# Kernel optimization log

Measured on AMD Instinct MI355X. Metric: run time of the kernel, lower is better.

The kernel has to match this reference:

```python
import jax, jax.numpy as jnp
import numpy as np

N, IN, HID, HEADS, OUT, E = 50000, 128, 64, 4, 128, 800000
NEG_SLOPE = 0.2


def _gat_conv(x, src, dst, W, a_src, a_dst, b, heads, ch, concat):
    # x: [N, F_in]; W: [F_in, heads*ch]; a_src/a_dst: [heads, ch]; b: [heads*ch] or [ch]
    n = x.shape[0]
    h = (x @ W).reshape(n, heads, ch)                       # [N,H,C]
    al_s = jnp.einsum('nhc,hc->nh', h, a_src)               # [N,H]
    al_d = jnp.einsum('nhc,hc->nh', h, a_dst)               # [N,H]
    e = jax.nn.leaky_relu(al_s[src] + al_d[dst], NEG_SLOPE)  # [E,H]
    # segment softmax over destination nodes (every node has a self-loop)
    m = jax.ops.segment_max(e, dst, num_segments=n)
    ex = jnp.exp(e - m[dst])
    denom = jax.ops.segment_sum(ex, dst, num_segments=n)
    alpha = ex / denom[dst]                                  # [E,H]
    msg = h[src] * alpha[:, :, None]                         # [E,H,C]
    out = jax.ops.segment_sum(msg, dst, num_segments=n)      # [N,H,C]
    out = out.reshape(n, heads * ch) if concat else out.mean(axis=1)
    return out + b


def setup_inputs() -> dict:
    key = jax.random.key(0)
    ks = jax.random.split(key, 10)
    s = 0.1
    return {
        'node_features': jax.random.normal(ks[0], (N, IN), jnp.float32),
        'edge_index': jax.random.randint(ks[1], (2, E), 0, N, jnp.int64),
        'W1': jax.random.normal(ks[2], (IN, HEADS * HID), jnp.float32) * s,
        'a1_src': jax.random.normal(ks[3], (HEADS, HID), jnp.float32) * s,
        'a1_dst': jax.random.normal(ks[4], (HEADS, HID), jnp.float32) * s,
        'b1': jnp.zeros((HEADS * HID,), jnp.float32),
        'W2': jax.random.normal(ks[5], (HEADS * HID, OUT), jnp.float32) * s,
        'a2_src': jax.random.normal(ks[6], (1, OUT), jnp.float32) * s,
        'a2_dst': jax.random.normal(ks[7], (1, OUT), jnp.float32) * s,
        'b2': jnp.zeros((OUT,), jnp.float32),
    }


def reference(node_features, edge_index, W1, a1_src, a1_dst, b1, W2, a2_src, a2_dst, b2):
    n = node_features.shape[0]
    loops = jnp.arange(n, dtype=edge_index.dtype)
    src = jnp.concatenate([edge_index[0], loops])  # PyG adds self-loops by default
    dst = jnp.concatenate([edge_index[1], loops])
    x = _gat_conv(node_features, src, dst, W1, a1_src, a1_dst, b1, HEADS, HID, True)
    x = jax.nn.relu(x)
    x = _gat_conv(x, src, dst, W2, a2_src, a2_dst, b2, 1, OUT, False)
    return x
```

## Files before the change

kernel.cpp:

```cpp
#include <hip/hip_runtime.h>
#include <math.h>

#define N_NODES 50000
#define F_IN    128
#define HIDC    64
#define HEADS   4
#define C1      (HEADS*HIDC)
#define F_OUT   128
#define NE      800000
#define NET     (NE + N_NODES)
#define NEG_SLOPE 0.2f

#define NPB   49
#define NBUCK 1021
#define BPAD  16
#define K4CAP 2048
#define SCHUNK 8192

typedef unsigned short ushort_t;
typedef signed char    schar_t;
typedef __attribute__((ext_vector_type(8))) short bf16x8;
typedef __attribute__((ext_vector_type(8))) unsigned short us8;
typedef __attribute__((ext_vector_type(4))) float f32x4;

__device__ __forceinline__ float b2f(ushort_t x) {
  return __uint_as_float(((unsigned int)x) << 16);
}
__device__ __forceinline__ ushort_t f2bf(float f) {
  unsigned int u = __float_as_uint(f);
  return (ushort_t)((u + 0x7fffu + ((u >> 16) & 1u)) >> 16);
}
__device__ __forceinline__ float u2f_lo(unsigned int u) { return __uint_as_float(u << 16); }
__device__ __forceinline__ float u2f_hi(unsigned int u) { return __uint_as_float(u & 0xffff0000u); }

__device__ __forceinline__ void fma8v(float ww, uint4 vv, float* a) {
  a[0] = fmaf(ww, u2f_lo(vv.x), a[0]); a[1] = fmaf(ww, u2f_hi(vv.x), a[1]);
  a[2] = fmaf(ww, u2f_lo(vv.y), a[2]); a[3] = fmaf(ww, u2f_hi(vv.y), a[3]);
  a[4] = fmaf(ww, u2f_lo(vv.z), a[4]); a[5] = fmaf(ww, u2f_hi(vv.z), a[5]);
  a[6] = fmaf(ww, u2f_lo(vv.w), a[6]); a[7] = fmaf(ww, u2f_hi(vv.w), a[7]);
}
__device__ __forceinline__ void fma8q(float wsc, uint2 vv, float* a) {
  int x = (int)vv.x, y = (int)vv.y;
  a[0] = fmaf(wsc, (float)(schar_t)(x),        a[0]);
  a[1] = fmaf(wsc, (float)(schar_t)(x >> 8),   a[1]);
  a[2] = fmaf(wsc, (float)(schar_t)(x >> 16),  a[2]);
  a[3] = fmaf(wsc, (float)(x >> 24),           a[3]);
  a[4] = fmaf(wsc, (float)(schar_t)(y),        a[4]);
  a[5] = fmaf(wsc, (float)(schar_t)(y >> 8),   a[5]);
  a[6] = fmaf(wsc, (float)(schar_t)(y >> 16),  a[6]);
  a[7] = fmaf(wsc, (float)(y >> 24),           a[7]);
}


__global__ __launch_bounds__(256) void bucket_count(const int* __restrict__ ei,
                                                    int* __restrict__ bcnt) {
  __shared__ int hist[NBUCK];
  for (int i = threadIdx.x; i < NBUCK; i += 256) hist[i] = 0;
  __syncthreads();
  int stride = gridDim.x * 256;
  for (int e = blockIdx.x * 256 + threadIdx.x; e < NET; e += stride) {
    int d = (e < NE) ? ei[NE + e] : (e - NE);
    atomicAdd(&hist[d / NPB], 1);
  }
  __syncthreads();
  for (int i = threadIdx.x; i < NBUCK; i += 256)
    if (hist[i]) atomicAdd(&bcnt[i * BPAD], hist[i]);
}

__global__ __launch_bounds__(1024) void scan_buckets(const int* __restrict__ bcnt,
                                                     int* __restrict__ boff) {
  __shared__ int sh[1024];
  int t = threadIdx.x;
  sh[t] = (t < NBUCK) ? bcnt[t * BPAD] : 0;
  __syncthreads();
#pragma unroll
  for (int off = 1; off < 1024; off <<= 1) {
    int u = (t >= off) ? sh[t - off] : 0;
    __syncthreads();
    sh[t] += u;
    __syncthreads();
  }
  if (t < NBUCK) boff[t + 1] = sh[t];
  if (t == 0) boff[0] = 0;
}

__global__ __launch_bounds__(1024) void bucket_scatter_blocked(const int* __restrict__ ei,
                                                               const int* __restrict__ boff,
                                                               int* __restrict__ bfill,
                                                               int2* __restrict__ pairs) {
  __shared__ int hist[NBUCK];
  __shared__ int gbase[NBUCK];
  __shared__ int fill[NBUCK];
  int c0 = blockIdx.x * SCHUNK;
  int cend = min(c0 + SCHUNK, NET);
  for (int i = threadIdx.x; i < NBUCK; i += 1024) { hist[i] = 0; fill[i] = 0; }
  __syncthreads();
  for (int e = c0 + threadIdx.x; e < cend; e += 1024) {
    int d = (e < NE) ? ei[NE + e] : (e - NE);
    atomicAdd(&hist[d / NPB], 1);
  }
  __syncthreads();
  for (int i = threadIdx.x; i < NBUCK; i += 1024)
    if (hist[i]) gbase[i] = boff[i] + atomicAdd(&bfill[i * BPAD], hist[i]);
  __syncthreads();
  for (int e = c0 + threadIdx.x; e < cend; e += 1024) {
    int s, d;
    if (e < NE) { s = ei[e]; d = ei[NE + e]; }
    else        { s = e - NE; d = s; }
    int b = d / NPB;
    int lpos = atomicAdd(&fill[b], 1);
    pairs[gbase[b] + lpos] = make_int2(s, d);
  }
}

__global__ __launch_bounds__(256) void build_csr(const int2* __restrict__ pairs,
                                                 const int* __restrict__ boff,
                                                 int* __restrict__ rowptr,
                                                 int* __restrict__ colsrc) {
  __shared__ int cnt[NPB];
  __shared__ int loc[NPB + 1];
  __shared__ int2 buf[K4CAP];
  int b = blockIdx.x, t = threadIdx.x;
  int p0 = boff[b], p1 = boff[b + 1];
  int m = p1 - p0;
  int n0 = b * NPB;
  int nn = min(NPB, N_NODES - n0);
  for (int i = t; i < NPB; i += 256) cnt[i] = 0;
  __syncthreads();
  bool inlds = (m <= K4CAP);
  for (int i = t; i < m; i += 256) {
    int2 p = pairs[p0 + i];
    if (inlds) buf[i] = p;
    atomicAdd(&cnt[p.y - n0], 1);
  }
  __syncthreads();
  if (t == 0) {
    int run = 0;
#pragma unroll 1
    for (int j = 0; j < nn; ++j) { loc[j] = run; run += cnt[j]; }
    loc[nn] = run;
  }
  __syncthreads();
  for (int j = t; j < nn; j += 256) rowptr[n0 + j] = p0 + loc[j];
  if (t == 0 && n0 + nn == N_NODES) rowptr[N_NODES] = NET;
  for (int i = t; i < NPB; i += 256) cnt[i] = 0;
  __syncthreads();
  for (int i = t; i < m; i += 256) {
    int2 p = inlds ? buf[i] : pairs[p0 + i];
    int j = p.y - n0;
    int pos = atomicAdd(&cnt[j], 1);
    colsrc[p0 + loc[j] + pos] = p.x;
  }
}


__global__ void transpose_both(const float* __restrict__ W1, ushort_t* __restrict__ W1t,
                               const float* __restrict__ W2, ushort_t* __restrict__ W2t) {
  int idx = blockIdx.x * blockDim.x + threadIdx.x;
  if (idx < F_IN * C1) {
    int k = idx / C1, n = idx - k * C1;
    W1t[(size_t)n * F_IN + k] = f2bf(W1[idx]);
  } else {
    int j = idx - F_IN * C1;
    if (j < C1 * F_OUT) {
      int k = j / F_OUT, n = j - k * F_OUT;
      W2t[(size_t)n * C1 + k] = f2bf(W2[j]);
    }
  }
}


#define BKS 64
#define LDT 72

__device__ __forceinline__ us8 stage8(const ushort_t* p) { return *(const us8*)p; }
__device__ __forceinline__ us8 stage8(const float* p) {
  float4 f0 = *(const float4*)p;
  float4 f1 = *(const float4*)(p + 4);
  us8 o;
  o[0] = f2bf(f0.x); o[1] = f2bf(f0.y); o[2] = f2bf(f0.z); o[3] = f2bf(f0.w);
  o[4] = f2bf(f1.x); o[5] = f2bf(f1.y); o[6] = f2bf(f1.z); o[7] = f2bf(f1.w);
  return o;
}

template<int K, int NCOL, int AL_MODE, typename AT, typename CT>
__global__ __launch_bounds__(256) void gemm_mfma(const AT* __restrict__ A,
                                                 const ushort_t* __restrict__ Bt,
                                                 CT* __restrict__ C,
                                                 float* __restrict__ scales,
                                                 const float* __restrict__ a_s,
                                                 const float* __restrict__ a_d,
                                                 float* __restrict__ als,
                                                 float* __restrict__ ald) {
  __shared__ __align__(16) char smem[2 * 128 * LDT * 2];
  ushort_t (*Asl)[LDT] = (ushort_t(*)[LDT])smem;
  ushort_t (*Bsl)[LDT] = (ushort_t(*)[LDT])(smem + 128 * LDT * 2);

  const int tid = threadIdx.x;
  const int lane = tid & 63;
  const int wave = tid >> 6;
  const int wr = wave >> 1, wc = wave & 1;
  const int row0 = blockIdx.y * 128;
  const int col0 = blockIdx.x * 128;
  const int l15 = lane & 15, l4 = lane >> 4;

  f32x4 acc[4][4] = {};

  for (int k0 = 0; k0 < K; k0 += BKS) {
#pragma unroll
    for (int i = 0; i < 4; ++i) {
      int seg = tid + i * 256;
      int row = seg >> 3, kq = (seg & 7) * 8;
      int arow = row0 + row;
      us8 v = {0, 0, 0, 0, 0, 0, 0, 0};
      if (arow < N_NODES) v = stage8(&A[(size_t)arow * K + k0 + kq]);
      *(us8*)&Asl[row][kq] = v;
    }
#pragma unroll
    for (int i = 0; i < 4; ++i) {
      int seg = tid + i * 256;
      int row = seg >> 3, kq = (seg & 7) * 8;
      us8 v = *(const us8*)&Bt[(size_t)(col0 + row) * K + k0 + kq];
      *(us8*)&Bsl[row][kq] = v;
    }
    __syncthreads();
#pragma unroll
    for (int kk = 0; kk < BKS; kk += 32) {
      bf16x8 af[4], bfr[4];
#pragma unroll
      for (int mi = 0; mi < 4; ++mi)
        af[mi] = *(const bf16x8*)&Asl[wr * 64 + mi * 16 + l15][kk + l4 * 8];
#pragma unroll
      for (int ni = 0; ni < 4; ++ni)
        bfr[ni] = *(const bf16x8*)&Bsl[wc * 64 + ni * 16 + l15][kk + l4 * 8];
#pragma unroll
      for (int mi = 0; mi < 4; ++mi)
#pragma unroll
        for (int ni = 0; ni < 4; ++ni)
          acc[mi][ni] = __builtin_amdgcn_mfma_f32_16x16x32_bf16(af[mi], bfr[ni], acc[mi][ni], 0, 0, 0);
    }
    __syncthreads();
  }

  {
    const int albase = (AL_MODE == 1 ? col0 : 0) + wc * 64;
    float asv[4], adv[4];
#pragma unroll
    for (int ni = 0; ni < 4; ++ni) {
      asv[ni] = a_s[albase + ni * 16 + l15];
      adv[ni] = a_d[albase + ni * 16 + l15];
    }
#pragma unroll
    for (int mi = 0; mi < 4; ++mi) {
      float ps[4], pd[4];
#pragma unroll
      for (int r = 0; r < 4; ++r) {
        ps[r] = acc[mi][0][r] * asv[0] + acc[mi][1][r] * asv[1] +
                acc[mi][2][r] * asv[2] + acc[mi][3][r] * asv[3];
        pd[r] = acc[mi][0][r] * adv[0] + acc[mi][1][r] * adv[1] +
                acc[mi][2][r] * adv[2] + acc[mi][3][r] * adv[3];
      }
#pragma unroll
      for (int m = 1; m < 16; m <<= 1) {
#pragma unroll
        for (int r = 0; r < 4; ++r) {
          ps[r] += __shfl_xor(ps[r], m, 64);
          pd[r] += __shfl_xor(pd[r], m, 64);
        }
      }
      if (l15 == 0) {
#pragma unroll
        for (int r = 0; r < 4; ++r) {
          int row = row0 + wr * 64 + mi * 16 + l4 * 4 + r;
          if (row < N_NODES) {
            if (AL_MODE == 1) {
              int h = albase >> 6;
              als[row * 4 + h] = ps[r];
              ald[row * 4 + h] = pd[r];
            } else {
              atomicAdd(&als[row], ps[r]);
              atomicAdd(&ald[row], pd[r]);
            }
          }
        }
      }
    }
  }

  {
    ushort_t (*Ep)[136] = (ushort_t(*)[136])smem;
#pragma unroll
    for (int mi = 0; mi < 4; ++mi)
#pragma unroll
      for (int ni = 0; ni < 4; ++ni)
#pragma unroll
        for (int r = 0; r < 4; ++r)
          Ep[wr * 64 + mi * 16 + l4 * 4 + r][wc * 64 + ni * 16 + l15] = f2bf(acc[mi][ni][r]);
    __syncthreads();
    int row = tid >> 1, half = tid & 1;
    int grow = row0 + row;
    if (grow < N_NODES) {
      if constexpr (sizeof(CT) == 1) {
        float vals[64];
        float amax = 0.f;
#pragma unroll
        for (int i = 0; i < 8; ++i) {
          us8 v = *(const us8*)&Ep[row][half * 64 + i * 8];
#pragma unroll
          for (int j = 0; j < 8; ++j) {
            float f = b2f((ushort_t)v[j]);
            vals[i * 8 + j] = f;
            amax = fmaxf(amax, fabsf(f));
          }
        }
        float inv = amax > 0.f ? 127.f / amax : 0.f;
        scales[grow * 4 + (col0 >> 6) + half] = amax * (1.f / 127.f);
        schar_t ob[64];
#pragma unroll
        for (int i = 0; i < 64; ++i)
          ob[i] = (schar_t)(int)rintf(vals[i] * inv);
#pragma unroll
        for (int i = 0; i < 4; ++i)
          *(us8*)&C[(size_t)grow * NCOL + col0 + half * 64 + i * 16] =
              *(const us8*)&ob[i * 16];
      } else {
#pragma unroll
        for (int i = 0; i < 8; ++i)
          *(us8*)&C[(size_t)grow * NCOL + col0 + half * 64 + i * 8] =
              *(const us8*)&Ep[row][half * 64 + i * 8];
      }
    }
  }
}


__global__ __launch_bounds__(256) void agg1(const int* __restrict__ rowptr,
                                            const int* __restrict__ colsrc,
                                            const schar_t* __restrict__ Hq,
                                            const float* __restrict__ Sc,
                                            const float* __restrict__ als,
                                            const float* __restrict__ ald,
                                            const float* __restrict__ b1,
                                            ushort_t* __restrict__ X2b) {
  int wave = threadIdx.x >> 6, lane = threadIdx.x & 63;
  int n = blockIdx.x * 4 + wave;
  if (n >= N_NODES) return;
  int half = lane >> 5, li = lane & 31, h = li >> 3;
  float ad = ald[n * 4 + h];
  int beg = rowptr[n], end = rowptr[n + 1];
  float a[8] = {};
  float s = 0.f;
  int i = beg + half;
  for (; i + 6 < end; i += 8) {
    int s0 = colsrc[i], s1 = colsrc[i + 2], s2 = colsrc[i + 4], s3 = colsrc[i + 6];
    float sc0 = als[s0 * 4 + h] + ad;
    float sc1 = als[s1 * 4 + h] + ad;
    float sc2 = als[s2 * 4 + h] + ad;
    float sc3 = als[s3 * 4 + h] + ad;
    float q0 = Sc[s0 * 4 + h], q1 = Sc[s1 * 4 + h], q2 = Sc[s2 * 4 + h], q3 = Sc[s3 * 4 + h];
    uint2 v0 = *(const uint2*)&Hq[(size_t)s0 * C1 + li * 8];
    uint2 v1 = *(const uint2*)&Hq[(size_t)s1 * C1 + li * 8];
    uint2 v2 = *(const uint2*)&Hq[(size_t)s2 * C1 + li * 8];
    uint2 v3 = *(const uint2*)&Hq[(size_t)s3 * C1 + li * 8];
    sc0 = sc0 > 0.f ? sc0 : NEG_SLOPE * sc0;
    sc1 = sc1 > 0.f ? sc1 : NEG_SLOPE * sc1;
    sc2 = sc2 > 0.f ? sc2 : NEG_SLOPE * sc2;
    sc3 = sc3 > 0.f ? sc3 : NEG_SLOPE * sc3;
    float w0 = __expf(sc0), w1 = __expf(sc1), w2 = __expf(sc2), w3 = __expf(sc3);
    s += (w0 + w1) + (w2 + w3);
    fma8q(w0 * q0, v0, a); fma8q(w1 * q1, v1, a);
    fma8q(w2 * q2, v2, a); fma8q(w3 * q3, v3, a);
  }
  for (; i + 2 < end; i += 4) {
    int s0 = colsrc[i], s1 = colsrc[i + 2];
    float sc0 = als[s0 * 4 + h] + ad;
    float sc1 = als[s1 * 4 + h] + ad;
    float q0 = Sc[s0 * 4 + h], q1 = Sc[s1 * 4 + h];
    uint2 v0 = *(const uint2*)&Hq[(size_t)s0 * C1 + li * 8];
    uint2 v1 = *(const uint2*)&Hq[(size_t)s1 * C1 + li * 8];
    sc0 = sc0 > 0.f ? sc0 : NEG_SLOPE * sc0;
    sc1 = sc1 > 0.f ? sc1 : NEG_SLOPE * sc1;
    float w0 = __expf(sc0), w1 = __expf(sc1);
    s += w0 + w1;
    fma8q(w0 * q0, v0, a); fma8q(w1 * q1, v1, a);
  }
  for (; i < end; i += 2) {
    int s0 = colsrc[i];
    float sc0 = als[s0 * 4 + h] + ad;
    float q0 = Sc[s0 * 4 + h];
    uint2 v0 = *(const uint2*)&Hq[(size_t)s0 * C1 + li * 8];
    sc0 = sc0 > 0.f ? sc0 : NEG_SLOPE * sc0;
    float w0 = __expf(sc0);
    s += w0;
    fma8q(w0 * q0, v0, a);
  }
#pragma unroll
  for (int j = 0; j < 8; ++j) a[j] += __shfl_xor(a[j], 32, 64);
  s += __shfl_xor(s, 32, 64);
  if (lane < 32) {
    float si = 1.f / s;
    int c = li * 8;
    float4 bb0 = *(const float4*)&b1[c];
    float4 bb1 = *(const float4*)&b1[c + 4];
    ushort_t o[8];
    o[0] = f2bf(fmaxf(a[0] * si + bb0.x, 0.f));
    o[1] = f2bf(fmaxf(a[1] * si + bb0.y, 0.f));
    o[2] = f2bf(fmaxf(a[2] * si + bb0.z, 0.f));
    o[3] = f2bf(fmaxf(a[3] * si + bb0.w, 0.f));
    o[4] = f2bf(fmaxf(a[4] * si + bb1.x, 0.f));
    o[5] = f2bf(fmaxf(a[5] * si + bb1.y, 0.f));
    o[6] = f2bf(fmaxf(a[6] * si + bb1.z, 0.f));
    o[7] = f2bf(fmaxf(a[7] * si + bb1.w, 0.f));
    *(us8*)&X2b[(size_t)n * C1 + c] = *(const us8*)o;
  }
}

__global__ __launch_bounds__(256) void agg2(const int* __restrict__ rowptr,
                                            const int* __restrict__ colsrc,
                                            const ushort_t* __restrict__ Hb,
                                            const float* __restrict__ als,
                                            const float* __restrict__ ald,
                                            const float* __restrict__ b2,
                                            float* __restrict__ out) {
  int wave = threadIdx.x >> 6, lane = threadIdx.x & 63;
  int n = blockIdx.x * 4 + wave;
  if (n >= N_NODES) return;
  int quarter = lane >> 4, li = lane & 15;
  float ad = ald[n];
  int beg = rowptr[n], end = rowptr[n + 1];
  float a[8] = {};
  float s = 0.f;
  int i = beg + quarter;
  for (; i + 12 < end; i += 16) {
    int s0 = colsrc[i], s1 = colsrc[i + 4], s2 = colsrc[i + 8], s3 = colsrc[i + 12];
    float sc0 = als[s0] + ad;
    float sc1 = als[s1] + ad;
    float sc2 = als[s2] + ad;
    float sc3 = als[s3] + ad;
    uint4 v0 = *(const uint4*)&Hb[(size_t)s0 * F_OUT + li * 8];
    uint4 v1 = *(const uint4*)&Hb[(size_t)s1 * F_OUT + li * 8];
    uint4 v2 = *(const uint4*)&Hb[(size_t)s2 * F_OUT + li * 8];
    uint4 v3 = *(const uint4*)&Hb[(size_t)s3 * F_OUT + li * 8];
    sc0 = sc0 > 0.f ? sc0 : NEG_SLOPE * sc0;
    sc1 = sc1 > 0.f ? sc1 : NEG_SLOPE * sc1;
    sc2 = sc2 > 0.f ? sc2 : NEG_SLOPE * sc2;
    sc3 = sc3 > 0.f ? sc3 : NEG_SLOPE * sc3;
    float w0 = __expf(sc0), w1 = __expf(sc1), w2 = __expf(sc2), w3 = __expf(sc3);
    s += (w0 + w1) + (w2 + w3);
    fma8v(w0, v0, a); fma8v(w1, v1, a); fma8v(w2, v2, a); fma8v(w3, v3, a);
  }
  for (; i + 4 < end; i += 8) {
    int s0 = colsrc[i], s1 = colsrc[i + 4];
    float sc0 = als[s0] + ad;
    float sc1 = als[s1] + ad;
    uint4 v0 = *(const uint4*)&Hb[(size_t)s0 * F_OUT + li * 8];
    uint4 v1 = *(const uint4*)&Hb[(size_t)s1 * F_OUT + li * 8];
    sc0 = sc0 > 0.f ? sc0 : NEG_SLOPE * sc0;
    sc1 = sc1 > 0.f ? sc1 : NEG_SLOPE * sc1;
    float w0 = __expf(sc0), w1 = __expf(sc1);
    s += w0 + w1;
    fma8v(w0, v0, a); fma8v(w1, v1, a);
  }
  for (; i < end; i += 4) {
    int s0 = colsrc[i];
    float sc0 = als[s0] + ad;
    uint4 v0 = *(const uint4*)&Hb[(size_t)s0 * F_OUT + li * 8];
    sc0 = sc0 > 0.f ? sc0 : NEG_SLOPE * sc0;
    float w0 = __expf(sc0);
    s += w0;
    fma8v(w0, v0, a);
  }
#pragma unroll
  for (int j = 0; j < 8; ++j) a[j] += __shfl_xor(a[j], 16, 64);
#pragma unroll
  for (int j = 0; j < 8; ++j) a[j] += __shfl_xor(a[j], 32, 64);
  s += __shfl_xor(s, 16, 64);
  s += __shfl_xor(s, 32, 64);
  if (lane < 16) {
    float si = 1.f / s;
    int c = li * 8;
    float4 bb0 = *(const float4*)&b2[c];
    float4 bb1 = *(const float4*)&b2[c + 4];
    float4 o0, o1;
    o0.x = a[0] * si + bb0.x; o0.y = a[1] * si + bb0.y;
    o0.z = a[2] * si + bb0.z; o0.w = a[3] * si + bb0.w;
    o1.x = a[4] * si + bb1.x; o1.y = a[5] * si + bb1.y;
    o1.z = a[6] * si + bb1.z; o1.w = a[7] * si + bb1.w;
    *(float4*)&out[(size_t)n * F_OUT + c] = o0;
    *(float4*)&out[(size_t)n * F_OUT + c + 4] = o1;
  }
}


extern "C" void kernel_launch(void* const* d_in, const int* in_sizes, int n_in,
                              void* d_out, int out_size, void* d_ws, size_t ws_size,
                              hipStream_t stream) {
  const float* X   = (const float*)d_in[0];
  const int*   EI  = (const int*)d_in[1];
  const float* W1  = (const float*)d_in[2];
  const float* a1s = (const float*)d_in[3];
  const float* a1d = (const float*)d_in[4];
  const float* b1  = (const float*)d_in[5];
  const float* W2  = (const float*)d_in[6];
  const float* a2s = (const float*)d_in[7];
  const float* a2d = (const float*)d_in[8];
  const float* b2  = (const float*)d_in[9];
  float* out = (float*)d_out;

  char* ws = (char*)d_ws;
  size_t off = 0;
  auto alloc = [&](size_t bytes) -> void* {
    void* p = ws + off;
    off += (bytes + 255) & ~(size_t)255;
    return p;
  };
  int* bcnt       = (int*)alloc((size_t)NBUCK * BPAD * 4);
  int* bfill      = (int*)alloc((size_t)NBUCK * BPAD * 4);
  float* ALS2     = (float*)alloc((size_t)N_NODES * 4);
  float* ALD2     = (float*)alloc((size_t)N_NODES * 4);
  size_t zero_span = off;
  int* boff       = (int*)alloc((size_t)(NBUCK + 1) * 4);
  int* rowptr     = (int*)alloc((size_t)(N_NODES + 1) * 4);
  int* colsrc     = (int*)alloc((size_t)NET * 4);
  int2* pairs     = (int2*)alloc((size_t)NET * 8);
  ushort_t* W1t   = (ushort_t*)alloc((size_t)C1 * F_IN * 2);
  ushort_t* W2t   = (ushort_t*)alloc((size_t)F_OUT * C1 * 2);
  schar_t* H1q    = (schar_t*)alloc((size_t)N_NODES * C1);
  float* SC1      = (float*)alloc((size_t)N_NODES * HEADS * 4);
  float* ALS1     = (float*)alloc((size_t)N_NODES * HEADS * 4);
  float* ALD1     = (float*)alloc((size_t)N_NODES * HEADS * 4);
  ushort_t* X2b   = (ushort_t*)alloc((size_t)N_NODES * C1 * 2);
  ushort_t* H2b = (ushort_t*)H1q;

  hipMemsetAsync(ws, 0, zero_span, stream);

  bucket_count<<<128, 256, 0, stream>>>(EI, bcnt);
  scan_buckets<<<1, 1024, 0, stream>>>(bcnt, boff);
  bucket_scatter_blocked<<<(NET + SCHUNK - 1) / SCHUNK, 1024, 0, stream>>>(EI, boff, bfill, pairs);
  build_csr<<<NBUCK, 256, 0, stream>>>(pairs, boff, rowptr, colsrc);

  transpose_both<<<(F_IN * C1 + C1 * F_OUT + 255) / 256, 256, 0, stream>>>(W1, W1t, W2, W2t);

  {
    dim3 grid(C1 / 128, (N_NODES + 127) / 128);
    gemm_mfma<F_IN, C1, 1, float, schar_t><<<grid, 256, 0, stream>>>(
        X, W1t, H1q, SC1, a1s, a1d, ALS1, ALD1);
  }
  agg1<<<(N_NODES + 3) / 4, 256, 0, stream>>>(rowptr, colsrc, H1q, SC1, ALS1, ALD1, b1, X2b);

  {
    dim3 grid(F_OUT / 128, (N_NODES + 127) / 128);
    gemm_mfma<C1, F_OUT, 2, ushort_t, ushort_t><<<grid, 256, 0, stream>>>(
        X2b, W2t, H2b, nullptr, a2s, a2d, ALS2, ALD2);
  }
  agg2<<<(N_NODES + 3) / 4, 256, 0, stream>>>(rowptr, colsrc, H2b, ALS2, ALD2, b2, out);
}
```

Before: 176.0 us.

## Quantize layer-2 features to int8 and widen per-lane gather to 16 bytes

The second GEMM now writes int8-quantized features with per-64-column scales instead of bf16, so agg2 gathers half as many bytes per edge. Both aggregation kernels are restructured so each lane loads 16 int8 values (uint4) per neighbor, with more edge groups per wave and an extra shuffle reduction stage. This cuts the gather bandwidth of the second aggregation and makes wider loads in the first. In exchange the layer-2 output carries int8 quantization error, and the extra reduction and register pressure may cost occupancy.

Result: slower. 194.9 us (+10.7%).

```diff
diff --git a/kernel.cpp b/kernel.cpp
--- a/kernel.cpp
+++ b/kernel.cpp
@@ -30,25 +30,25 @@
   unsigned int u = __float_as_uint(f);
   return (ushort_t)((u + 0x7fffu + ((u >> 16) & 1u)) >> 16);
 }
-__device__ __forceinline__ float u2f_lo(unsigned int u) { return __uint_as_float(u << 16); }
-__device__ __forceinline__ float u2f_hi(unsigned int u) { return __uint_as_float(u & 0xffff0000u); }
-
-__device__ __forceinline__ void fma8v(float ww, uint4 vv, float* a) {
-  a[0] = fmaf(ww, u2f_lo(vv.x), a[0]); a[1] = fmaf(ww, u2f_hi(vv.x), a[1]);
-  a[2] = fmaf(ww, u2f_lo(vv.y), a[2]); a[3] = fmaf(ww, u2f_hi(vv.y), a[3]);
-  a[4] = fmaf(ww, u2f_lo(vv.z), a[4]); a[5] = fmaf(ww, u2f_hi(vv.z), a[5]);
-  a[6] = fmaf(ww, u2f_lo(vv.w), a[6]); a[7] = fmaf(ww, u2f_hi(vv.w), a[7]);
-}
-__device__ __forceinline__ void fma8q(float wsc, uint2 vv, float* a) {
-  int x = (int)vv.x, y = (int)vv.y;
-  a[0] = fmaf(wsc, (float)(schar_t)(x),        a[0]);
-  a[1] = fmaf(wsc, (float)(schar_t)(x >> 8),   a[1]);
-  a[2] = fmaf(wsc, (float)(schar_t)(x >> 16),  a[2]);
-  a[3] = fmaf(wsc, (float)(x >> 24),           a[3]);
-  a[4] = fmaf(wsc, (float)(schar_t)(y),        a[4]);
-  a[5] = fmaf(wsc, (float)(schar_t)(y >> 8),   a[5]);
-  a[6] = fmaf(wsc, (float)(schar_t)(y >> 16),  a[6]);
-  a[7] = fmaf(wsc, (float)(y >> 24),           a[7]);
+
+__device__ __forceinline__ void fma16q(float wsc, uint4 vv, float* a) {
+  int p0 = (int)vv.x, p1 = (int)vv.y, p2 = (int)vv.z, p3 = (int)vv.w;
+  a[0]  = fmaf(wsc, (float)(schar_t)(p0),       a[0]);
+  a[1]  = fmaf(wsc, (float)(schar_t)(p0 >> 8),  a[1]);
+  a[2]  = fmaf(wsc, (float)(schar_t)(p0 >> 16), a[2]);
+  a[3]  = fmaf(wsc, (float)(p0 >> 24),          a[3]);
+  a[4]  = fmaf(wsc, (float)(schar_t)(p1),       a[4]);
+  a[5]  = fmaf(wsc, (float)(schar_t)(p1 >> 8),  a[5]);
+  a[6]  = fmaf(wsc, (float)(schar_t)(p1 >> 16), a[6]);
+  a[7]  = fmaf(wsc, (float)(p1 >> 24),          a[7]);
+  a[8]  = fmaf(wsc, (float)(schar_t)(p2),       a[8]);
+  a[9]  = fmaf(wsc, (float)(schar_t)(p2 >> 8),  a[9]);
+  a[10] = fmaf(wsc, (float)(schar_t)(p2 >> 16), a[10]);
+  a[11] = fmaf(wsc, (float)(p2 >> 24),          a[11]);
+  a[12] = fmaf(wsc, (float)(schar_t)(p3),       a[12]);
+  a[13] = fmaf(wsc, (float)(schar_t)(p3 >> 8),  a[13]);
+  a[14] = fmaf(wsc, (float)(schar_t)(p3 >> 16), a[14]);
+  a[15] = fmaf(wsc, (float)(p3 >> 24),          a[15]);
 }
 
 
@@ -183,7 +183,7 @@
   return o;
 }
 
-template<int K, int NCOL, int AL_MODE, typename AT, typename CT>
+template<int K, int NCOL, int AL_MODE, int SCST, typename AT, typename CT>
 __global__ __launch_bounds__(256) void gemm_mfma(const AT* __restrict__ A,
                                                  const ushort_t* __restrict__ Bt,
                                                  CT* __restrict__ C,
@@ -314,7 +314,7 @@
           }
         }
         float inv = amax > 0.f ? 127.f / amax : 0.f;
-        scales[grow * 4 + (col0 >> 6) + half] = amax * (1.f / 127.f);
+        scales[grow * SCST + (col0 >> 6) + half] = amax * (1.f / 127.f);
         schar_t ob[64];
 #pragma unroll
         for (int i = 0; i < 64; ++i)
@@ -345,79 +345,78 @@
   int wave = threadIdx.x >> 6, lane = threadIdx.x & 63;
   int n = blockIdx.x * 4 + wave;
   if (n >= N_NODES) return;
-  int half = lane >> 5, li = lane & 31, h = li >> 3;
+  int grp = lane >> 4, li = lane & 15;
+  int h = li >> 2;
   float ad = ald[n * 4 + h];
   int beg = rowptr[n], end = rowptr[n + 1];
-  float a[8] = {};
+  float a[16] = {};
   float s = 0.f;
-  int i = beg + half;
-  for (; i + 6 < end; i += 8) {
-    int s0 = colsrc[i], s1 = colsrc[i + 2], s2 = colsrc[i + 4], s3 = colsrc[i + 6];
+  int i = beg + grp;
+  for (; i + 12 < end; i += 16) {
+    int s0 = colsrc[i], s1 = colsrc[i + 4], s2 = colsrc[i + 8], s3 = colsrc[i + 12];
     float sc0 = als[s0 * 4 + h] + ad;
     float sc1 = als[s1 * 4 + h] + ad;
     float sc2 = als[s2 * 4 + h] + ad;
     float sc3 = als[s3 * 4 + h] + ad;
     float q0 = Sc[s0 * 4 + h], q1 = Sc[s1 * 4 + h], q2 = Sc[s2 * 4 + h], q3 = Sc[s3 * 4 + h];
-    uint2 v0 = *(const uint2*)&Hq[(size_t)s0 * C1 + li * 8];
-    uint2 v1 = *(const uint2*)&Hq[(size_t)s1 * C1 + li * 8];
-    uint2 v2 = *(const uint2*)&Hq[(size_t)s2 * C1 + li * 8];
-    uint2 v3 = *(const uint2*)&Hq[(size_t)s3 * C1 + li * 8];
+    uint4 v0 = *(const uint4*)&Hq[(size_t)s0 * C1 + li * 16];
+    uint4 v1 = *(const uint4*)&Hq[(size_t)s1 * C1 + li * 16];
+    uint4 v2 = *(const uint4*)&Hq[(size_t)s2 * C1 + li * 16];
+    uint4 v3 = *(const uint4*)&Hq[(size_t)s3 * C1 + li * 16];
     sc0 = sc0 > 0.f ? sc0 : NEG_SLOPE * sc0;
     sc1 = sc1 > 0.f ? sc1 : NEG_SLOPE * sc1;
     sc2 = sc2 > 0.f ? sc2 : NEG_SLOPE * sc2;
     sc3 = sc3 > 0.f ? sc3 : NEG_SLOPE * sc3;
     float w0 = __expf(sc0), w1 = __expf(sc1), w2 = __expf(sc2), w3 = __expf(sc3);
     s += (w0 + w1) + (w2 + w3);
-    fma8q(w0 * q0, v0, a); fma8q(w1 * q1, v1, a);
-    fma8q(w2 * q2, v2, a); fma8q(w3 * q3, v3, a);
-  }
-  for (; i + 2 < end; i += 4) {
-    int s0 = colsrc[i], s1 = colsrc[i + 2];
+    fma16q(w0 * q0, v0, a); fma16q(w1 * q1, v1, a);
+    fma16q(w2 * q2, v2, a); fma16q(w3 * q3, v3, a);
+  }
+  for (; i + 4 < end; i += 8) {
+    int s0 = colsrc[i], s1 = colsrc[i + 4];
     float sc0 = als[s0 * 4 + h] + ad;
     float sc1 = als[s1 * 4 + h] + ad;
     float q0 = Sc[s0 * 4 + h], q1 = Sc[s1 * 4 + h];
-    uint2 v0 = *(const uint2*)&Hq[(size_t)s0 * C1 + li * 8];
-    uint2 v1 = *(const uint2*)&Hq[(size_t)s1 * C1 + li * 8];
+    uint4 v0 = *(const uint4*)&Hq[(size_t)s0 * C1 + li * 16];
+    uint4 v1 = *(const uint4*)&Hq[(size_t)s1 * C1 + li * 16];
     sc0 = sc0 > 0.f ? sc0 : NEG_SLOPE * sc0;
     sc1 = sc1 > 0.f ? sc1 : NEG_SLOPE * sc1;
     float w0 = __expf(sc0), w1 = __expf(sc1);
     s += w0 + w1;
-    fma8q(w0 * q0, v0, a); fma8q(w1 * q1, v1, a);
-  }
-  for (; i < end; i += 2) {
+    fma16q(w0 * q0, v0, a); fma16q(w1 * q1, v1, a);
+  }
+  for (; i < end; i += 4) {
     int s0 = colsrc[i];
     float sc0 = als[s0 * 4 + h] + ad;
     float q0 = Sc[s0 * 4 + h];
-    uint2 v0 = *(const uint2*)&Hq[(size_t)s0 * C1 + li * 8];
+    uint4 v0 = *(const uint4*)&Hq[(size_t)s0 * C1 + li * 16];
     sc0 = sc0 > 0.f ? sc0 : NEG_SLOPE * sc0;
     float w0 = __expf(sc0);
     s += w0;
-    fma8q(w0 * q0, v0, a);
-  }
-#pragma unroll
-  for (int j = 0; j < 8; ++j) a[j] += __shfl_xor(a[j], 32, 64);
+    fma16q(w0 * q0, v0, a);
+  }
+#pragma unroll
+  for (int j = 0; j < 16; ++j) a[j] += __shfl_xor(a[j], 16, 64);
+#pragma unroll
+  for (int j = 0; j < 16; ++j) a[j] += __shfl_xor(a[j], 32, 64);
+  s += __shfl_xor(s, 16, 64);
   s += __shfl_xor(s, 32, 64);
-  if (lane < 32) {
+  if (lane < 16) {
     float si = 1.f / s;
-    int c = li * 8;
-    float4 bb0 = *(const float4*)&b1[c];
-    float4 bb1 = *(const float4*)&b1[c + 4];
-    ushort_t o[8];
-    o[0] = f2bf(fmaxf(a[0] * si + bb0.x, 0.f));
-    o[1] = f2bf(fmaxf(a[1] * si + bb0.y, 0.f));
-    o[2] = f2bf(fmaxf(a[2] * si + bb0.z, 0.f));
-    o[3] = f2bf(fmaxf(a[3] * si + bb0.w, 0.f));
-    o[4] = f2bf(fmaxf(a[4] * si + bb1.x, 0.f));
-    o[5] = f2bf(fmaxf(a[5] * si + bb1.y, 0.f));
-    o[6] = f2bf(fmaxf(a[6] * si + bb1.z, 0.f));
-    o[7] = f2bf(fmaxf(a[7] * si + bb1.w, 0.f));
-    *(us8*)&X2b[(size_t)n * C1 + c] = *(const us8*)o;
+    int c = li * 16;
+    ushort_t o[16];
+#pragma unroll
+    for (int j = 0; j < 16; ++j)
+      o[j] = f2bf(fmaxf(a[j] * si + b1[c + j], 0.f));
+    *(us8*)&X2b[(size_t)n * C1 + c] = *(const us8*)&o[0];
+    *(us8*)&X2b[(size_t)n * C1 + c + 8] = *(const us8*)&o[8];
   }
 }
 
 __global__ __launch_bounds__(256) void agg2(const int* __restrict__ rowptr,
                                             const int* __restrict__ colsrc,
-                                            const ushort_t* __restrict__ Hb,
+                                            const schar_t* __restrict__ Hq,
+                                            const float* __restrict__ Sc,
                                             const float* __restrict__ als,
                                             const float* __restrict__ ald,
                                             const float* __restrict__ b2,
@@ -425,69 +424,57 @@
   int wave = threadIdx.x >> 6, lane = threadIdx.x & 63;
   int n = blockIdx.x * 4 + wave;
   if (n >= N_NODES) return;
-  int quarter = lane >> 4, li = lane & 15;
+  int grp = lane >> 3, li = lane & 7;
+  int hb = li >> 2;
   float ad = ald[n];
   int beg = rowptr[n], end = rowptr[n + 1];
-  float a[8] = {};
+  float a[16] = {};
   float s = 0.f;
-  int i = beg + quarter;
-  for (; i + 12 < end; i += 16) {
-    int s0 = colsrc[i], s1 = colsrc[i + 4], s2 = colsrc[i + 8], s3 = colsrc[i + 12];
+  int i = beg + grp;
+  for (; i + 8 < end; i += 16) {
+    int s0 = colsrc[i], s1 = colsrc[i + 8];
     float sc0 = als[s0] + ad;
     float sc1 = als[s1] + ad;
-    float sc2 = als[s2] + ad;
-    float sc3 = als[s3] + ad;
-    uint4 v0 = *(const uint4*)&Hb[(size_t)s0 * F_OUT + li * 8];
-    uint4 v1 = *(const uint4*)&Hb[(size_t)s1 * F_OUT + li * 8];
-    uint4 v2 = *(const uint4*)&Hb[(size_t)s2 * F_OUT + li * 8];
-    uint4 v3 = *(const uint4*)&Hb[(size_t)s3 * F_OUT + li * 8];
-    sc0 = sc0 > 0.f ? sc0 : NEG_SLOPE * sc0;
-    sc1 = sc1 > 0.f ? sc1 : NEG_SLOPE * sc1;
-    sc2 = sc2 > 0.f ? sc2 : NEG_SLOPE * sc2;
-    sc3 = sc3 > 0.f ? sc3 : NEG_SLOPE * sc3;
-    float w0 = __expf(sc0), w1 = __expf(sc1), w2 = __expf(sc2), w3 = __expf(sc3);
-    s += (w0 + w1) + (w2 + w3);
-    fma8v(w0, v0, a); fma8v(w1, v1, a); fma8v(w2, v2, a); fma8v(w3, v3, a);
-  }
-  for (; i + 4 < end; i += 8) {
-    int s0 = colsrc[i], s1 = colsrc[i + 4];
-    float sc0 = als[s0] + ad;
-    float sc1 = als[s1] + ad;
-    uint4 v0 = *(const uint4*)&Hb[(size_t)s0 * F_OUT + li * 8];
-    uint4 v1 = *(const uint4*)&Hb[(size_t)s1 * F_OUT + li * 8];
+    float q0 = Sc[s0 * 2 + hb], q1 = Sc[s1 * 2 + hb];
+    uint4 v0 = *(const uint4*)&Hq[(size_t)s0 * F_OUT + li * 16];
+    uint4 v1 = *(const uint4*)&Hq[(size_t)s1 * F_OUT + li * 16];
     sc0 = sc0 > 0.f ? sc0 : NEG_SLOPE * sc0;
     sc1 = sc1 > 0.f ? sc1 : NEG_SLOPE * sc1;
     float w0 = __expf(sc0), w1 = __expf(sc1);
     s += w0 + w1;
-    fma8v(w0, v0, a); fma8v(w1, v1, a);
-  }
-  for (; i < end; i += 4) {
+    fma16q(w0 * q0, v0, a); fma16q(w1 * q1, v1, a);
+  }
+  for (; i < end; i += 8) {
     int s0 = colsrc[i];
     float sc0 = als[s0] + ad;
-    uint4 v0 = *(const uint4*)&Hb[(size_t)s0 * F_OUT + li * 8];
+    float q0 = Sc[s0 * 2 + hb];
+    uint4 v0 = *(const uint4*)&Hq[(size_t)s0 * F_OUT + li * 16];
     sc0 = sc0 > 0.f ? sc0 : NEG_SLOPE * sc0;
     float w0 = __expf(sc0);
     s += w0;
-    fma8v(w0, v0, a);
-  }
-#pragma unroll
-  for (int j = 0; j < 8; ++j) a[j] += __shfl_xor(a[j], 16, 64);
-#pragma unroll
-  for (int j = 0; j < 8; ++j) a[j] += __shfl_xor(a[j], 32, 64);
+    fma16q(w0 * q0, v0, a);
+  }
+#pragma unroll
+  for (int j = 0; j < 16; ++j) a[j] += __shfl_xor(a[j], 8, 64);
+#pragma unroll
+  for (int j = 0; j < 16; ++j) a[j] += __shfl_xor(a[j], 16, 64);
+#pragma unroll
+  for (int j = 0; j < 16; ++j) a[j] += __shfl_xor(a[j], 32, 64);
+  s += __shfl_xor(s, 8, 64);
   s += __shfl_xor(s, 16, 64);
   s += __shfl_xor(s, 32, 64);
-  if (lane < 16) {
+  if (lane < 8) {
     float si = 1.f / s;
-    int c = li * 8;
-    float4 bb0 = *(const float4*)&b2[c];
-    float4 bb1 = *(const float4*)&b2[c + 4];
-    float4 o0, o1;
-    o0.x = a[0] * si + bb0.x; o0.y = a[1] * si + bb0.y;
-    o0.z = a[2] * si + bb0.z; o0.w = a[3] * si + bb0.w;
-    o1.x = a[4] * si + bb1.x; o1.y = a[5] * si + bb1.y;
-    o1.z = a[6] * si + bb1.z; o1.w = a[7] * si + bb1.w;
-    *(float4*)&out[(size_t)n * F_OUT + c] = o0;
-    *(float4*)&out[(size_t)n * F_OUT + c + 4] = o1;
+    int c = li * 16;
+#pragma unroll
+    for (int j = 0; j < 4; ++j) {
+      float4 o;
+      o.x = a[j * 4 + 0] * si + b2[c + j * 4 + 0];
+      o.y = a[j * 4 + 1] * si + b2[c + j * 4 + 1];
+      o.z = a[j * 4 + 2] * si + b2[c + j * 4 + 2];
+      o.w = a[j * 4 + 3] * si + b2[c + j * 4 + 3];
+      *(float4*)&out[(size_t)n * F_OUT + c + j * 4] = o;
+    }
   }
 }
 
@@ -527,10 +514,11 @@
   ushort_t* W2t   = (ushort_t*)alloc((size_t)F_OUT * C1 * 2);
   schar_t* H1q    = (schar_t*)alloc((size_t)N_NODES * C1);
   float* SC1      = (float*)alloc((size_t)N_NODES * HEADS * 4);
+  float* SC2      = (float*)alloc((size_t)N_NODES * 2 * 4);
   float* ALS1     = (float*)alloc((size_t)N_NODES * HEADS * 4);
   float* ALD1     = (float*)alloc((size_t)N_NODES * HEADS * 4);
   ushort_t* X2b   = (ushort_t*)alloc((size_t)N_NODES * C1 * 2);
-  ushort_t* H2b = (ushort_t*)H1q;
+  schar_t* H2q = H1q;
 
   hipMemsetAsync(ws, 0, zero_span, stream);
 
@@ -543,15 +531,15 @@
 
   {
     dim3 grid(C1 / 128, (N_NODES + 127) / 128);
-    gemm_mfma<F_IN, C1, 1, float, schar_t><<<grid, 256, 0, stream>>>(
+    gemm_mfma<F_IN, C1, 1, 4, float, schar_t><<<grid, 256, 0, stream>>>(
         X, W1t, H1q, SC1, a1s, a1d, ALS1, ALD1);
   }
   agg1<<<(N_NODES + 3) / 4, 256, 0, stream>>>(rowptr, colsrc, H1q, SC1, ALS1, ALD1, b1, X2b);
 
   {
     dim3 grid(F_OUT / 128, (N_NODES + 127) / 128);
-    gemm_mfma<C1, F_OUT, 2, ushort_t, ushort_t><<<grid, 256, 0, stream>>>(
-        X2b, W2t, H2b, nullptr, a2s, a2d, ALS2, ALD2);
-  }
-  agg2<<<(N_NODES + 3) / 4, 256, 0, stream>>>(rowptr, colsrc, H2b, ALS2, ALD2, b2, out);
-}
+    gemm_mfma<C1, F_OUT, 2, 2, ushort_t, schar_t><<<grid, 256, 0, stream>>>(
+        X2b, W2t, H2q, SC2, a2s, a2d, ALS2, ALD2);
+  }
+  agg2<<<(N_NODES + 3) / 4, 256, 0, stream>>>(rowptr, colsrc, H2q, SC2, ALS2, ALD2, b2, out);
+}
```
